# Kernel tuning notes

Measured on AMD Instinct MI355X. Metric: run time of the kernel, lower is better.

Reference implementation:

```python
import jax, jax.numpy as jnp
import numpy as np

B, N, C, H = 16, 4096, 256, 4
D = C // H


def setup_inputs() -> dict:
    key = jax.random.key(0)
    ks = jax.random.split(key, 16)
    s = 0.02
    inp = {
        "x": jax.random.normal(ks[0], (B, N, C), jnp.float32),
        "encoding": jax.random.normal(ks[1], (2, B, 1, N, D), jnp.float32),
        "Wqkv_w": jax.random.normal(ks[2], (3 * C, C), jnp.float32) * s,
        "Wqkv_b": jnp.zeros((3 * C,), jnp.float32),
        "tssa_qkv_w": jax.random.normal(ks[3], (C, C), jnp.float32) * s,
        "tssa_qkv_b": jnp.zeros((C,), jnp.float32),
        "temp": jnp.ones((H, 1), jnp.float32),
        "tssa_out_w": jax.random.normal(ks[4], (C, C), jnp.float32) * s,
        "tssa_out_b": jnp.zeros((C,), jnp.float32),
        "out_proj_w": jax.random.normal(ks[5], (C, C), jnp.float32) * s,
        "out_proj_b": jnp.zeros((C,), jnp.float32),
        "ffn1_w": jax.random.normal(ks[6], (2 * C, 2 * C), jnp.float32) * s,
        "ffn1_b": jnp.zeros((2 * C,), jnp.float32),
        "ln_g": jnp.ones((2 * C,), jnp.float32),
        "ln_b": jnp.zeros((2 * C,), jnp.float32),
        "ffn2_w": jax.random.normal(ks[7], (C, 2 * C), jnp.float32) * s,
        "ffn2_b": jnp.zeros((C,), jnp.float32),
    }
    return inp


def _rotate_half(t):
    # (..., d) -> pairwise rotate: (x1, x2) -> (-x2, x1)
    t2 = t.reshape(t.shape[:-1] + (-1, 2))
    x1, x2 = t2[..., 0], t2[..., 1]
    return jnp.stack((-x2, x1), axis=-1).reshape(t.shape)


def reference(x, encoding, Wqkv_w, Wqkv_b, tssa_qkv_w, tssa_qkv_b, temp,
              tssa_out_w, tssa_out_b, out_proj_w, out_proj_b,
              ffn1_w, ffn1_b, ln_g, ln_b, ffn2_w, ffn2_b):
    b, n, c = x.shape
    h, d = H, D
    # QKV projection, layout (h, d, 3) on last dim as in unflatten(-1,(h,-1,3))
    qkv = (x @ Wqkv_w.T + Wqkv_b).reshape(b, n, h, d, 3).transpose(0, 2, 1, 3, 4)  # b h n d 3
    q, k, v = qkv[..., 0], qkv[..., 1], qkv[..., 2]
    rope = lambda t: t * encoding[0] + _rotate_half(t) * encoding[1]
    q = rope(q)
    k = rope(k)
    flat = lambda t: t.transpose(0, 2, 1, 3).reshape(b, n, c)  # b h n d -> b n (h d)
    w_input = (flat(q) + flat(k) + flat(v)) / 3.0
    # TSSA attention
    w = (w_input @ tssa_qkv_w.T + tssa_qkv_b).reshape(b, n, h, d).transpose(0, 2, 1, 3)  # b h n d
    norm = jnp.sqrt(jnp.sum(w * w, axis=2, keepdims=True))  # L2 over sequence axis N
    w_normed = w / jnp.maximum(norm, 1e-12)
    sum_ws = jnp.sum(w_normed * w_normed, axis=-1)  # b h n
    Pi = jax.nn.softmax(sum_ws * temp[None, :, :], axis=1)  # softmax over heads
    Pi_norm = Pi / (jnp.sum(Pi, axis=-1, keepdims=True) + 1e-8)
    dots = jnp.einsum('bhn,bhnd->bh', Pi_norm, w * w)  # (b,h,1,d) summed over d
    attn = 1.0 / (1.0 + dots)  # b h
    out = -(w * Pi[..., None]) * attn[:, :, None, None]  # b h n d
    out = out.transpose(0, 2, 1, 3).reshape(b, n, c)
    context = out @ tssa_out_w.T + tssa_out_b
    message = context @ out_proj_w.T + out_proj_b
    # residual FFN
    cat = jnp.concatenate([x, message], axis=-1)  # b n 2c
    h1 = cat @ ffn1_w.T + ffn1_b
    mu = jnp.mean(h1, axis=-1, keepdims=True)
    var = jnp.mean((h1 - mu) ** 2, axis=-1, keepdims=True)
    ln = (h1 - mu) / jnp.sqrt(var + 1e-5) * ln_g + ln_b
    g = jax.nn.gelu(ln, approximate=False)
    return x + (g @ ffn2_w.T + ffn2_b)
```

## Files before the change

### kernel.cpp

```cpp
#include <hip/hip_runtime.h>
#include <math.h>

#define Bc 16
#define Nc 4096

typedef __attribute__((ext_vector_type(8))) short short8;
typedef __attribute__((ext_vector_type(4))) float floatx4;

__device__ __forceinline__ unsigned short f2bf(float f) {
    union { float f; unsigned int u; } v; v.f = f;
    unsigned int u = v.u;
    return (unsigned short)((u + 0x7fffu + ((u >> 16) & 1u)) >> 16);
}
__device__ __forceinline__ float bf2f(unsigned short u) {
    union { unsigned int u; float f; } v; v.u = ((unsigned int)u) << 16;
    return v.f;
}

__device__ __forceinline__ void gll16(const unsigned short* g, unsigned short* l) {
    __builtin_amdgcn_global_load_lds(
        (const __attribute__((address_space(1))) void*)g,
        (__attribute__((address_space(3))) void*)l,
        16, 0, 0);
}

template <int EPI, typename TOUT>
__global__ __launch_bounds__(512) void gemm_bf(
    const unsigned short* __restrict__ A0, int lda0,
    const unsigned short* __restrict__ A1, int lda1, int K0,
    const unsigned short* __restrict__ W,
    const float* __restrict__ bias,
    const unsigned short* __restrict__ resid_bf,
    const float* __restrict__ Pi,
    const float* __restrict__ attnb,
    float* __restrict__ norm2,
    float* __restrict__ rowstats,
    const float* __restrict__ enc,
    const float* __restrict__ lng,
    const float* __restrict__ lnb,
    TOUT* __restrict__ C, int N, int K)
{
    __shared__ alignas(16) unsigned short As[128 * 64];
    __shared__ alignas(16) unsigned short Bs[256 * 64];

    const int t = threadIdx.x;
    const int bn = blockIdx.x, bm = blockIdx.y;
    const int lane = t & 63, wave = t >> 6;
    const int wm = wave >> 2, wn = wave & 3;
    const int quad = lane >> 4, l16 = lane & 15;
    const int rt = t >> 3, st = t & 7;

    floatx4 acc[4][4];
    #pragma unroll
    for (int i = 0; i < 4; ++i)
        #pragma unroll
        for (int j = 0; j < 4; ++j)
            acc[i][j] = (floatx4){0.f, 0.f, 0.f, 0.f};

    for (int k0 = 0; k0 < K; k0 += 64) {
        #pragma unroll
        for (int hh = 0; hh < 2; ++hh) {
            const int row = hh * 64 + rt;
            const int col = k0 + (st ^ (row & 7)) * 8;
            unsigned short* ldsa = As + row * 64 + st * 8;
            const size_t grow = (size_t)bm * 128 + row;
            if constexpr (EPI == 2) {
                const int b = (int)(grow >> 12);
                const int hd = col >> 6;
                const float sc = -Pi[grow * 4 + hd] * attnb[b * 4 + hd];
                const short8 a = *(const short8*)(A0 + grow * (size_t)lda0 + col);
                short8 o;
                #pragma unroll
                for (int j = 0; j < 8; ++j) o[j] = (short)f2bf(bf2f((unsigned short)a[j]) * sc);
                *(short8*)ldsa = o;
            } else if constexpr (EPI == 3) {
                const float2 stv = *(const float2*)(rowstats + grow * 2);
                const float mean = stv.x * (1.f / 512.f);
                const float rstd = rsqrtf(stv.y * (1.f / 512.f) - mean * mean + 1e-5f);
                const short8 a = *(const short8*)(A0 + grow * (size_t)lda0 + col);
                const float4 g0 = *(const float4*)(lng + col);
                const float4 g1 = *(const float4*)(lng + col + 4);
                const float4 bb0 = *(const float4*)(lnb + col);
                const float4 bb1 = *(const float4*)(lnb + col + 4);
                const float vg[8] = {g0.x, g0.y, g0.z, g0.w, g1.x, g1.y, g1.z, g1.w};
                const float vb[8] = {bb0.x, bb0.y, bb0.z, bb0.w, bb1.x, bb1.y, bb1.z, bb1.w};
                short8 o;
                #pragma unroll
                for (int jj = 0; jj < 8; ++jj) {
                    const float ln = (bf2f((unsigned short)a[jj]) - mean) * rstd * vg[jj] + vb[jj];
                    o[jj] = (short)f2bf(0.5f * ln * (1.f + erff(ln * 0.70710678118654752f)));
                }
                *(short8*)ldsa = o;
            } else {
                const unsigned short* src = (col < K0)
                    ? (A0 + grow * (size_t)lda0 + col)
                    : (A1 + grow * (size_t)lda1 + (col - K0));
                gll16(src, ldsa);
            }
        }
        #pragma unroll
        for (int hh = 0; hh < 4; ++hh) {
            const int row = hh * 64 + rt;
            const int col = k0 + (st ^ (row & 7)) * 8;
            gll16(W + ((size_t)bn * 256 + row) * (size_t)K + col, Bs + row * 64 + st * 8);
        }
        __syncthreads();
        #pragma unroll
        for (int kk = 0; kk < 2; ++kk) {
            short8 af[4], wf[4];
            #pragma unroll
            for (int i = 0; i < 4; ++i) {
                const int ra = wm * 64 + i * 16 + l16;
                af[i] = *(const short8*)(As + ra * 64 + ((quad + kk * 4) ^ (ra & 7)) * 8);
                const int rw = wn * 64 + i * 16 + l16;
                wf[i] = *(const short8*)(Bs + rw * 64 + ((quad + kk * 4) ^ (rw & 7)) * 8);
            }
            #pragma unroll
            for (int mi = 0; mi < 4; ++mi)
                #pragma unroll
                for (int ni = 0; ni < 4; ++ni)
                    acc[mi][ni] = __builtin_amdgcn_mfma_f32_16x16x32_bf16(
                        wf[ni], af[mi], acc[mi][ni], 0, 0, 0);
        }
        __syncthreads();
    }

    float rs[4], rq[4];
    if constexpr (EPI == 4) {
        #pragma unroll
        for (int m = 0; m < 4; ++m) { rs[m] = 0.f; rq[m] = 0.f; }
    }

    #pragma unroll
    for (int mi = 0; mi < 4; ++mi) {
        const size_t row = (size_t)bm * 128 + wm * 64 + mi * 16 + l16;
        #pragma unroll
        for (int ni = 0; ni < 4; ++ni) {
            const int cb = bn * 256 + wn * 64 + ni * 16 + quad * 4;
            const float4 b4 = *(const float4*)(bias + cb);
            if constexpr (EPI == 5) {
                const float s0 = acc[mi][ni][0] + b4.x;
                const float v0 = acc[mi][ni][1] + b4.y;
                const float s1 = acc[mi][ni][2] + b4.z;
                const float v1 = acc[mi][ni][3] + b4.w;
                const int j = cb >> 1;
                const int d = j & 63;
                const float2 e0 = *(const float2*)(enc + row * 64 + d);
                const float2 e1 = *(const float2*)(enc + 4194304 + row * 64 + d);
                const float r0 = s0 * e0.x - s1 * e1.x;
                const float r1 = s1 * e0.y + s0 * e1.y;
                ushort2 o;
                o.x = f2bf((r0 + v0) * (1.f / 3.f));
                o.y = f2bf((r1 + v1) * (1.f / 3.f));
                *(ushort2*)((unsigned short*)C + row * (size_t)N + j) = o;
            } else {
                float v[4] = {acc[mi][ni][0] + b4.x, acc[mi][ni][1] + b4.y,
                              acc[mi][ni][2] + b4.z, acc[mi][ni][3] + b4.w};
                if constexpr (EPI == 3) {
                    const ushort4 xr = *(const ushort4*)(resid_bf + row * (size_t)N + cb);
                    v[0] += bf2f(xr.x); v[1] += bf2f(xr.y);
                    v[2] += bf2f(xr.z); v[3] += bf2f(xr.w);
                }
                if constexpr (EPI == 4) {
                    #pragma unroll
                    for (int rg = 0; rg < 4; ++rg) { rs[mi] += v[rg]; rq[mi] += v[rg] * v[rg]; }
                }
                if constexpr (EPI == 1) {
                    float cs[4];
                    #pragma unroll
                    for (int rg = 0; rg < 4; ++rg) cs[rg] = v[rg] * v[rg];
                    #pragma unroll
                    for (int rg = 0; rg < 4; ++rg) {
                        float s = cs[rg];
                        s += __shfl_xor(s, 1, 64);
                        s += __shfl_xor(s, 2, 64);
                        s += __shfl_xor(s, 4, 64);
                        s += __shfl_xor(s, 8, 64);
                        if (l16 == 0) atomicAdd(&norm2[(bm >> 5) * 256 + cb + rg], s);
                    }
                }
                if constexpr (__is_same(TOUT, float)) {
                    float4 o; o.x = v[0]; o.y = v[1]; o.z = v[2]; o.w = v[3];
                    *(float4*)(C + row * (size_t)N + cb) = o;
                } else {
                    ushort4 o;
                    o.x = f2bf(v[0]); o.y = f2bf(v[1]); o.z = f2bf(v[2]); o.w = f2bf(v[3]);
                    *(ushort4*)(C + row * (size_t)N + cb) = o;
                }
            }
        }
    }
    if constexpr (EPI == 4) {
        #pragma unroll
        for (int mi = 0; mi < 4; ++mi) {
            float s = rs[mi], q = rq[mi];
            s += __shfl_xor(s, 16, 64); s += __shfl_xor(s, 32, 64);
            q += __shfl_xor(q, 16, 64); q += __shfl_xor(q, 32, 64);
            if (quad == 0) {
                const size_t row = (size_t)bm * 128 + wm * 64 + mi * 16 + l16;
                atomicAdd(&rowstats[row * 2], s);
                atomicAdd(&rowstats[row * 2 + 1], q);
            }
        }
    }
}

__device__ __forceinline__ void conv8(const float* src, unsigned short* dst, int i) {
    const float4 f0 = *(const float4*)(src + (size_t)i * 8);
    const float4 f1 = *(const float4*)(src + (size_t)i * 8 + 4);
    short8 sv;
    sv[0] = (short)f2bf(f0.x); sv[1] = (short)f2bf(f0.y);
    sv[2] = (short)f2bf(f0.z); sv[3] = (short)f2bf(f0.w);
    sv[4] = (short)f2bf(f1.x); sv[5] = (short)f2bf(f1.y);
    sv[6] = (short)f2bf(f1.z); sv[7] = (short)f2bf(f1.w);
    *(short8*)(dst + (size_t)i * 8) = sv;
}

__global__ __launch_bounds__(256) void prep_all(
    const float* __restrict__ x, const float* __restrict__ Wqkv,
    const float* __restrict__ bqkv, const float* __restrict__ tssa_w,
    const float* __restrict__ op_w, const float* __restrict__ to_w,
    const float* __restrict__ to_b, const float* __restrict__ op_b,
    const float* __restrict__ f1w, const float* __restrict__ f2w,
    unsigned short* __restrict__ x_bf, unsigned short* __restrict__ Wsv,
    float* __restrict__ bsv, unsigned short* __restrict__ tssa_bf,
    unsigned short* __restrict__ Wf, float* __restrict__ bfb,
    unsigned short* __restrict__ ffn1_bf, unsigned short* __restrict__ ffn2_bf,
    float* __restrict__ zbase, float* __restrict__ rowstats)
{
    const int blk = blockIdx.x, tt = threadIdx.x;
    if (blk < 8192) {
        conv8(x, x_bf, blk * 256 + tt);
    } else if (blk < 8704) {
        const int r = blk - 8192, c = tt;
        const int j = r >> 1;
        const int h = j >> 6, dd = j & 63;
        const int base = h * 192 + dd * 3;
        if (!(r & 1)) {
            Wsv[r * 256 + c] = f2bf(Wqkv[(base + 0) * 256 + c] + Wqkv[(base + 1) * 256 + c]);
            if (c == 0) bsv[r] = bqkv[base] + bqkv[base + 1];
        } else {
            Wsv[r * 256 + c] = f2bf(Wqkv[(base + 2) * 256 + c]);
            if (c == 0) bsv[r] = bqkv[base + 2];
        }
    } else if (blk < 8960) {
        const int i = blk - 8704;
        float s = 0.f;
        for (int k = 0; k < 256; ++k) s += op_w[i * 256 + k] * to_w[k * 256 + tt];
        Wf[i * 256 + tt] = f2bf(s);
    } else if (blk == 8960) {
        float s = op_b[tt];
        for (int k = 0; k < 256; ++k) s += op_w[tt * 256 + k] * to_b[k];
        bfb[tt] = s;
    } else if (blk < 8993) {
        conv8(tssa_w, tssa_bf, (blk - 8961) * 256 + tt);
    } else if (blk < 9121) {
        conv8(f1w, ffn1_bf, (blk - 8993) * 256 + tt);
    } else if (blk < 9185) {
        conv8(f2w, ffn2_bf, (blk - 9121) * 256 + tt);
    } else {
        const int i = (blk - 9185) * 256 + tt;
        if (i < 4288) zbase[i] = 0.f;
        else if (i < 135360) rowstats[i - 4288] = 0.f;
    }
}

__global__ __launch_bounds__(256) void pi_kernel(const unsigned short* __restrict__ w,
                                                 const float* __restrict__ norm2,
                                                 const float* __restrict__ temp,
                                                 float* __restrict__ Pi,
                                                 float* __restrict__ S,
                                                 float* __restrict__ T) {
    const int t = threadIdx.x;
    const int i = t & 15;
    const int lr = t >> 4;
    const size_t r = (size_t)blockIdx.x * 16 + lr;
    const int b = (int)(r >> 12);
    const unsigned short* wrow = w + r * 256;
    const float* n2row = norm2 + b * 256;
    float raw[4], nrm[4];
    #pragma unroll
    for (int h = 0; h < 4; ++h) {
        const ushort4 wv = *(const ushort4*)(wrow + h * 64 + i * 4);
        const float w0 = bf2f(wv.x), w1 = bf2f(wv.y), w2 = bf2f(wv.z), w3 = bf2f(wv.w);
        const float4 n2 = *(const float4*)(n2row + h * 64 + i * 4);
        const float s0 = w0 * w0, s1 = w1 * w1, s2 = w2 * w2, s3 = w3 * w3;
        raw[h] = s0 + s1 + s2 + s3;
        nrm[h] = s0 / fmaxf(n2.x, 1e-24f) + s1 / fmaxf(n2.y, 1e-24f)
               + s2 / fmaxf(n2.z, 1e-24f) + s3 / fmaxf(n2.w, 1e-24f);
    }
    #pragma unroll
    for (int off = 1; off < 16; off <<= 1) {
        #pragma unroll
        for (int h = 0; h < 4; ++h) {
            raw[h] += __shfl_xor(raw[h], off, 64);
            nrm[h] += __shfl_xor(nrm[h], off, 64);
        }
    }
    float sw[4], m = -1e30f;
    #pragma unroll
    for (int h = 0; h < 4; ++h) { sw[h] = nrm[h] * temp[h]; m = fmaxf(m, sw[h]); }
    float e[4], Z = 0.f;
    #pragma unroll
    for (int h = 0; h < 4; ++h) { e[h] = expf(sw[h] - m); Z += e[h]; }
    const float invZ = 1.f / Z;
    float pi[4];
    #pragma unroll
    for (int h = 0; h < 4; ++h) pi[h] = e[h] * invZ;
    if (i < 4) Pi[r * 4 + i] = pi[i];

    __shared__ float sS[16][4], sT[16][4];
    if (i == 0) {
        #pragma unroll
        for (int h = 0; h < 4; ++h) { sS[lr][h] = pi[h]; sT[lr][h] = pi[h] * raw[h]; }
    }
    __syncthreads();
    if (t < 4) {
        float as = 0.f, at = 0.f;
        for (int rr = 0; rr < 16; ++rr) { as += sS[rr][t]; at += sT[rr][t]; }
        atomicAdd(&S[b * 4 + t], as);
        atomicAdd(&T[b * 4 + t], at);
    }
}

__global__ void attn_kernel(const float* __restrict__ S, const float* __restrict__ T,
                            float* __restrict__ attn) {
    const int i = threadIdx.x;
    const float dots = T[i] / (S[i] + 1e-8f);
    attn[i] = 1.f / (1.f + dots);
}

extern "C" void kernel_launch(void* const* d_in, const int* in_sizes, int n_in,
                              void* d_out, int out_size, void* d_ws, size_t ws_size,
                              hipStream_t stream) {
    (void)in_sizes; (void)n_in; (void)out_size; (void)ws_size;
    const float* x          = (const float*)d_in[0];
    const float* enc        = (const float*)d_in[1];
    const float* Wqkv_w     = (const float*)d_in[2];
    const float* Wqkv_b     = (const float*)d_in[3];
    const float* tssa_qkv_w = (const float*)d_in[4];
    const float* tssa_qkv_b = (const float*)d_in[5];
    const float* temp       = (const float*)d_in[6];
    const float* tssa_out_w = (const float*)d_in[7];
    const float* tssa_out_b = (const float*)d_in[8];
    const float* out_proj_w = (const float*)d_in[9];
    const float* out_proj_b = (const float*)d_in[10];
    const float* ffn1_w     = (const float*)d_in[11];
    const float* ffn1_b     = (const float*)d_in[12];
    const float* ln_g       = (const float*)d_in[13];
    const float* ln_b       = (const float*)d_in[14];
    const float* ffn2_w     = (const float*)d_in[15];
    const float* ffn2_b     = (const float*)d_in[16];
    float* outp = (float*)d_out;

    const int M = Bc * Nc;

    char* ws = (char*)d_ws;
    unsigned short* x_bf  = (unsigned short*)(ws);
    unsigned short* wi_bf = (unsigned short*)(ws + (size_t)(32 << 20));
    unsigned short* h1_bf = (unsigned short*)(ws + (size_t)(32 << 20));
    unsigned short* w_bf  = (unsigned short*)(ws + (size_t)(64 << 20));
    unsigned short* msg_bf= (unsigned short*)(ws + (size_t)(96 << 20));
    float* fb    = (float*)(ws + (size_t)(128 << 20));
    float* Pi    = fb;
    float* norm2 = Pi + 262144;
    float* Sb    = norm2 + 4096;
    float* Tb    = Sb + 64;
    float* attnb = Tb + 64;
    float* bsv   = attnb + 64;
    float* bfb   = bsv + 512;
    float* rowstats = bfb + 256;
    unsigned short* Wsv_bf  = (unsigned short*)(rowstats + 131072);
    unsigned short* tssa_bf = Wsv_bf + 131072;
    unsigned short* Wf_bf   = tssa_bf + 65536;
    unsigned short* ffn1_bf = Wf_bf + 65536;
    unsigned short* ffn2_bf = ffn1_bf + 262144;

    prep_all<<<9714, 256, 0, stream>>>(
        x, Wqkv_w, Wqkv_b, tssa_qkv_w, out_proj_w, tssa_out_w, tssa_out_b,
        out_proj_b, ffn1_w, ffn2_w,
        x_bf, Wsv_bf, bsv, tssa_bf, Wf_bf, bfb, ffn1_bf, ffn2_bf,
        norm2, rowstats);

    gemm_bf<5, unsigned short><<<dim3(2, M / 128), 512, 0, stream>>>(
        x_bf, 256, x_bf, 256, 256, Wsv_bf, bsv,
        nullptr, nullptr, nullptr, nullptr, nullptr,
        enc, nullptr, nullptr, wi_bf, 256, 256);

    gemm_bf<1, unsigned short><<<dim3(1, M / 128), 512, 0, stream>>>(
        wi_bf, 256, wi_bf, 256, 256, tssa_bf, tssa_qkv_b,
        nullptr, nullptr, nullptr, norm2, nullptr,
        nullptr, nullptr, nullptr, w_bf, 256, 256);

    pi_kernel<<<4096, 256, 0, stream>>>(w_bf, norm2, temp, Pi, Sb, Tb);
    attn_kernel<<<1, 64, 0, stream>>>(Sb, Tb, attnb);

    gemm_bf<2, unsigned short><<<dim3(1, M / 128), 512, 0, stream>>>(
        w_bf, 256, w_bf, 256, 256, Wf_bf, bfb,
        nullptr, Pi, attnb, nullptr, nullptr,
        nullptr, nullptr, nullptr, msg_bf, 256, 256);

    gemm_bf<4, unsigned short><<<dim3(2, M / 128), 512, 0, stream>>>(
        x_bf, 256, msg_bf, 256, 256, ffn1_bf, ffn1_b,
        nullptr, nullptr, nullptr, nullptr, rowstats,
        nullptr, nullptr, nullptr, h1_bf, 512, 512);

    gemm_bf<3, float><<<dim3(1, M / 128), 512, 0, stream>>>(
        h1_bf, 512, h1_bf, 512, 512, ffn2_bf, ffn2_b,
        x_bf, nullptr, nullptr, nullptr, rowstats,
        nullptr, ln_g, ln_b, outp, 256, 512);
}
```

Measured before the change: 471.7 us.

## Double-buffer GEMM LDS tiles with software prefetch and fast GELU

Restructures the shared GEMM main loop into a double-buffered pipeline. The next K-tile's global-to-LDS loads, or register prefetches for the transforming epilogues, are issued before computing the current tile, with explicit vmcnt/lgkmcnt waits and barriers. K becomes a compile-time template parameter so the loop fully unrolls. It also hoists the LayerNorm row statistics out of the loop and replaces erff with an Abramowitz-Stegun polynomial GELU, which lowers the transform cost but adds small approximation error and doubles LDS use, which may reduce occupancy.

```diff
diff --git a/kernel.cpp b/kernel.cpp
--- a/kernel.cpp
+++ b/kernel.cpp
@@ -6,6 +6,11 @@
 
 typedef __attribute__((ext_vector_type(8))) short short8;
 typedef __attribute__((ext_vector_type(4))) float floatx4;
+
+#define VMWAIT(n) asm volatile("s_waitcnt vmcnt(" #n ")" ::: "memory")
+#define LGKM0     asm volatile("s_waitcnt lgkmcnt(0)" ::: "memory")
+#define CFENCE    asm volatile("" ::: "memory")
+#define BARRIER   __builtin_amdgcn_s_barrier()
 
 __device__ __forceinline__ unsigned short f2bf(float f) {
     union { float f; unsigned int u; } v; v.f = f;
@@ -15,6 +20,17 @@
 __device__ __forceinline__ float bf2f(unsigned short u) {
     union { unsigned int u; float f; } v; v.u = ((unsigned int)u) << 16;
     return v.f;
+}
+
+__device__ __forceinline__ float gelu_f(float x) {
+    const float z = x * 0.70710678118654752f;
+    const float az = fabsf(z);
+    const float t = 1.f / (1.f + 0.3275911f * az);
+    const float poly = t * (0.254829592f + t * (-0.284496736f +
+                       t * (1.421413741f + t * (-1.453152027f + t * 1.061405429f))));
+    const float e = __expf(-z * z);
+    const float er = copysignf(1.f - poly * e, z);
+    return 0.5f * x * (1.f + er);
 }
 
 __device__ __forceinline__ void gll16(const unsigned short* g, unsigned short* l) {
@@ -24,7 +40,7 @@
         16, 0, 0);
 }
 
-template <int EPI, typename TOUT>
+template <int EPI, int KT, typename TOUT>
 __global__ __launch_bounds__(512) void gemm_bf(
     const unsigned short* __restrict__ A0, int lda0,
     const unsigned short* __restrict__ A1, int lda1, int K0,
@@ -38,10 +54,12 @@
     const float* __restrict__ enc,
     const float* __restrict__ lng,
     const float* __restrict__ lnb,
-    TOUT* __restrict__ C, int N, int K)
+    TOUT* __restrict__ C, int N)
 {
-    __shared__ alignas(16) unsigned short As[128 * 64];
-    __shared__ alignas(16) unsigned short Bs[256 * 64];
+    constexpr int NT = KT / 64;
+    constexpr bool REG = (EPI == 2) || (EPI == 3);
+    __shared__ alignas(16) unsigned short As[2 * 128 * 64];
+    __shared__ alignas(16) unsigned short Bs[2 * 256 * 64];
 
     const int t = threadIdx.x;
     const int bn = blockIdx.x, bm = blockIdx.y;
@@ -50,6 +68,20 @@
     const int quad = lane >> 4, l16 = lane & 15;
     const int rt = t >> 3, st = t & 7;
 
+    const int swz = (st ^ (rt & 7)) * 8;
+    const size_t g0 = (size_t)bm * 128 + rt;
+    const size_t g1 = g0 + 64;
+
+    float mean0 = 0.f, rstd0 = 0.f, mean1 = 0.f, rstd1 = 0.f;
+    if constexpr (EPI == 3) {
+        const float2 s0 = *(const float2*)(rowstats + g0 * 2);
+        const float2 s1 = *(const float2*)(rowstats + g1 * 2);
+        mean0 = s0.x * (1.f / 512.f);
+        rstd0 = rsqrtf(s0.y * (1.f / 512.f) - mean0 * mean0 + 1e-5f);
+        mean1 = s1.x * (1.f / 512.f);
+        rstd1 = rsqrtf(s1.y * (1.f / 512.f) - mean1 * mean1 + 1e-5f);
+    }
+
     floatx4 acc[4][4];
     #pragma unroll
     for (int i = 0; i < 4; ++i)
@@ -57,63 +89,73 @@
         for (int j = 0; j < 4; ++j)
             acc[i][j] = (floatx4){0.f, 0.f, 0.f, 0.f};
 
-    for (int k0 = 0; k0 < K; k0 += 64) {
-        #pragma unroll
-        for (int hh = 0; hh < 2; ++hh) {
-            const int row = hh * 64 + rt;
-            const int col = k0 + (st ^ (row & 7)) * 8;
-            unsigned short* ldsa = As + row * 64 + st * 8;
-            const size_t grow = (size_t)bm * 128 + row;
-            if constexpr (EPI == 2) {
-                const int b = (int)(grow >> 12);
-                const int hd = col >> 6;
-                const float sc = -Pi[grow * 4 + hd] * attnb[b * 4 + hd];
-                const short8 a = *(const short8*)(A0 + grow * (size_t)lda0 + col);
-                short8 o;
-                #pragma unroll
-                for (int j = 0; j < 8; ++j) o[j] = (short)f2bf(bf2f((unsigned short)a[j]) * sc);
-                *(short8*)ldsa = o;
-            } else if constexpr (EPI == 3) {
-                const float2 stv = *(const float2*)(rowstats + grow * 2);
-                const float mean = stv.x * (1.f / 512.f);
-                const float rstd = rsqrtf(stv.y * (1.f / 512.f) - mean * mean + 1e-5f);
-                const short8 a = *(const short8*)(A0 + grow * (size_t)lda0 + col);
-                const float4 g0 = *(const float4*)(lng + col);
-                const float4 g1 = *(const float4*)(lng + col + 4);
-                const float4 bb0 = *(const float4*)(lnb + col);
-                const float4 bb1 = *(const float4*)(lnb + col + 4);
-                const float vg[8] = {g0.x, g0.y, g0.z, g0.w, g1.x, g1.y, g1.z, g1.w};
-                const float vb[8] = {bb0.x, bb0.y, bb0.z, bb0.w, bb1.x, bb1.y, bb1.z, bb1.w};
-                short8 o;
-                #pragma unroll
-                for (int jj = 0; jj < 8; ++jj) {
-                    const float ln = (bf2f((unsigned short)a[jj]) - mean) * rstd * vg[jj] + vb[jj];
-                    o[jj] = (short)f2bf(0.5f * ln * (1.f + erff(ln * 0.70710678118654752f)));
-                }
-                *(short8*)ldsa = o;
-            } else {
-                const unsigned short* src = (col < K0)
-                    ? (A0 + grow * (size_t)lda0 + col)
-                    : (A1 + grow * (size_t)lda1 + (col - K0));
-                gll16(src, ldsa);
-            }
-        }
-        #pragma unroll
-        for (int hh = 0; hh < 4; ++hh) {
-            const int row = hh * 64 + rt;
-            const int col = k0 + (st ^ (row & 7)) * 8;
-            gll16(W + ((size_t)bn * 256 + row) * (size_t)K + col, Bs + row * 64 + st * 8);
-        }
-        __syncthreads();
+    auto stageW = [&](int buf, int tt) {
+        unsigned short* dst = Bs + buf * (256 * 64) + rt * 64 + st * 8;
+        const unsigned short* src = W + ((size_t)bn * 256 + rt) * KT + tt * 64 + swz;
+        #pragma unroll
+        for (int hh = 0; hh < 4; ++hh)
+            gll16(src + (size_t)hh * 64 * KT, dst + hh * 64 * 64);
+    };
+    auto stageA = [&](int buf, int tt) {
+        const int col = tt * 64 + swz;
+        unsigned short* dst = As + buf * (128 * 64) + rt * 64 + st * 8;
+        const unsigned short* p0 = (col < K0) ? (A0 + g0 * (size_t)lda0 + col)
+                                              : (A1 + g0 * (size_t)lda1 + (col - K0));
+        const unsigned short* p1 = (col < K0) ? (A0 + g1 * (size_t)lda0 + col)
+                                              : (A1 + g1 * (size_t)lda1 + (col - K0));
+        gll16(p0, dst);
+        gll16(p1, dst + 64 * 64);
+    };
+    auto loadA = [&](int tt, short8& r0, short8& r1) {
+        const int col = tt * 64 + swz;
+        r0 = *(const short8*)(A0 + g0 * (size_t)lda0 + col);
+        r1 = *(const short8*)(A0 + g1 * (size_t)lda0 + col);
+    };
+    auto xformWrite = [&](int buf, int tt, short8 r0, short8 r1) {
+        unsigned short* d0 = As + buf * (128 * 64) + rt * 64 + st * 8;
+        unsigned short* d1 = d0 + 64 * 64;
+        if constexpr (EPI == 2) {
+            const float asc = attnb[((bm >> 5) << 2) + tt];
+            const float sc0 = -Pi[g0 * 4 + tt] * asc;
+            const float sc1 = -Pi[g1 * 4 + tt] * asc;
+            short8 o0, o1;
+            #pragma unroll
+            for (int j = 0; j < 8; ++j) {
+                o0[j] = (short)f2bf(bf2f((unsigned short)r0[j]) * sc0);
+                o1[j] = (short)f2bf(bf2f((unsigned short)r1[j]) * sc1);
+            }
+            *(short8*)d0 = o0; *(short8*)d1 = o1;
+        } else {
+            const int col = tt * 64 + swz;
+            const float4 ga = *(const float4*)(lng + col);
+            const float4 gb = *(const float4*)(lng + col + 4);
+            const float4 ba = *(const float4*)(lnb + col);
+            const float4 bb = *(const float4*)(lnb + col + 4);
+            const float vg[8] = {ga.x, ga.y, ga.z, ga.w, gb.x, gb.y, gb.z, gb.w};
+            const float vb[8] = {ba.x, ba.y, ba.z, ba.w, bb.x, bb.y, bb.z, bb.w};
+            short8 o0, o1;
+            #pragma unroll
+            for (int j = 0; j < 8; ++j) {
+                const float l0 = (bf2f((unsigned short)r0[j]) - mean0) * rstd0 * vg[j] + vb[j];
+                const float l1 = (bf2f((unsigned short)r1[j]) - mean1) * rstd1 * vg[j] + vb[j];
+                o0[j] = (short)f2bf(gelu_f(l0));
+                o1[j] = (short)f2bf(gelu_f(l1));
+            }
+            *(short8*)d0 = o0; *(short8*)d1 = o1;
+        }
+    };
+    auto compute = [&](int buf) {
+        const unsigned short* Ab = As + buf * (128 * 64);
+        const unsigned short* Bb = Bs + buf * (256 * 64);
         #pragma unroll
         for (int kk = 0; kk < 2; ++kk) {
             short8 af[4], wf[4];
             #pragma unroll
             for (int i = 0; i < 4; ++i) {
                 const int ra = wm * 64 + i * 16 + l16;
-                af[i] = *(const short8*)(As + ra * 64 + ((quad + kk * 4) ^ (ra & 7)) * 8);
+                af[i] = *(const short8*)(Ab + ra * 64 + ((quad + kk * 4) ^ (ra & 7)) * 8);
                 const int rw = wn * 64 + i * 16 + l16;
-                wf[i] = *(const short8*)(Bs + rw * 64 + ((quad + kk * 4) ^ (rw & 7)) * 8);
+                wf[i] = *(const short8*)(Bb + rw * 64 + ((quad + kk * 4) ^ (rw & 7)) * 8);
             }
             #pragma unroll
             for (int mi = 0; mi < 4; ++mi)
@@ -122,7 +164,52 @@
                     acc[mi][ni] = __builtin_amdgcn_mfma_f32_16x16x32_bf16(
                         wf[ni], af[mi], acc[mi][ni], 0, 0, 0);
         }
-        __syncthreads();
+    };
+
+    short8 pa0, pa1;
+    if constexpr (REG) {
+        short8 c0, c1;
+        loadA(0, c0, c1);
+        CFENCE;
+        stageW(0, 0);
+        CFENCE;
+        loadA(1, pa0, pa1);
+        CFENCE;
+        VMWAIT(6);
+        xformWrite(0, 0, c0, c1);
+    } else {
+        stageA(0, 0);
+        stageW(0, 0);
+        CFENCE;
+    }
+
+    int cur = 0;
+    #pragma unroll
+    for (int tt = 0; tt < NT; ++tt) {
+        const int nxt = cur ^ 1;
+        if (tt + 1 < NT) {
+            if constexpr (!REG) stageA(nxt, tt + 1);
+            stageW(nxt, tt + 1);
+            CFENCE;
+            VMWAIT(6);
+        } else {
+            VMWAIT(0);
+        }
+        LGKM0;
+        BARRIER;
+        if constexpr (REG) {
+            if (tt + 1 < NT) {
+                VMWAIT(4);
+                xformWrite(nxt, tt + 1, pa0, pa1);
+                if (tt + 2 < NT) { CFENCE; loadA(tt + 2, pa0, pa1); CFENCE; }
+            }
+        }
+        compute(cur);
+        if (tt + 1 < NT) {
+            LGKM0;
+            BARRIER;
+        }
+        cur = nxt;
     }
 
     float rs[4], rq[4];
@@ -382,31 +469,31 @@
         x_bf, Wsv_bf, bsv, tssa_bf, Wf_bf, bfb, ffn1_bf, ffn2_bf,
         norm2, rowstats);
 
-    gemm_bf<5, unsigned short><<<dim3(2, M / 128), 512, 0, stream>>>(
+    gemm_bf<5, 256, unsigned short><<<dim3(2, M / 128), 512, 0, stream>>>(
         x_bf, 256, x_bf, 256, 256, Wsv_bf, bsv,
         nullptr, nullptr, nullptr, nullptr, nullptr,
-        enc, nullptr, nullptr, wi_bf, 256, 256);
-
-    gemm_bf<1, unsigned short><<<dim3(1, M / 128), 512, 0, stream>>>(
+        enc, nullptr, nullptr, wi_bf, 256);
+
+    gemm_bf<1, 256, unsigned short><<<dim3(1, M / 128), 512, 0, stream>>>(
         wi_bf, 256, wi_bf, 256, 256, tssa_bf, tssa_qkv_b,
         nullptr, nullptr, nullptr, norm2, nullptr,
-        nullptr, nullptr, nullptr, w_bf, 256, 256);
+        nullptr, nullptr, nullptr, w_bf, 256);
 
     pi_kernel<<<4096, 256, 0, stream>>>(w_bf, norm2, temp, Pi, Sb, Tb);
     attn_kernel<<<1, 64, 0, stream>>>(Sb, Tb, attnb);
 
-    gemm_bf<2, unsigned short><<<dim3(1, M / 128), 512, 0, stream>>>(
+    gemm_bf<2, 256, unsigned short><<<dim3(1, M / 128), 512, 0, stream>>>(
         w_bf, 256, w_bf, 256, 256, Wf_bf, bfb,
         nullptr, Pi, attnb, nullptr, nullptr,
-        nullptr, nullptr, nullptr, msg_bf, 256, 256);
-
-    gemm_bf<4, unsigned short><<<dim3(2, M / 128), 512, 0, stream>>>(
+        nullptr, nullptr, nullptr, msg_bf, 256);
+
+    gemm_bf<4, 512, unsigned short><<<dim3(2, M / 128), 512, 0, stream>>>(
         x_bf, 256, msg_bf, 256, 256, ffn1_bf, ffn1_b,
         nullptr, nullptr, nullptr, nullptr, rowstats,
-        nullptr, nullptr, nullptr, h1_bf, 512, 512);
-
-    gemm_bf<3, float><<<dim3(1, M / 128), 512, 0, stream>>>(
+        nullptr, nullptr, nullptr, h1_bf, 512);
+
+    gemm_bf<3, 512, float><<<dim3(1, M / 128), 512, 0, stream>>>(
         h1_bf, 512, h1_bf, 512, 512, ffn2_bf, ffn2_b,
         x_bf, nullptr, nullptr, nullptr, rowstats,
-        nullptr, ln_g, ln_b, outp, 256, 512);
-}
+        nullptr, ln_g, ln_b, outp, 256);
+}
```

After: 547.1 us. +16.0%, slower.
